# Kernel optimization log

Measured on AMD Instinct MI355X. Metric: run time of the kernel, lower is better.

The kernel has to match this reference:

```python
import jax, jax.numpy as jnp
import numpy as np

B, T, D, H, Dh, ROT = 2, 2048, 2048, 16, 128, 64
DFF = 4 * D
EPS = 1e-5
NEG = -1e9


def setup_inputs() -> dict:
    key = jax.random.key(0)
    ks = jax.random.split(key, 8)
    s = lambda k, shape, sc: jax.random.normal(k, shape, jnp.float32) * sc
    return {
        "x": s(ks[0], (B, T, D), 1.0),
        "ln_scale": jnp.ones((D,), jnp.float32),
        "ln_offset": jnp.zeros((D,), jnp.float32),
        "wq": s(ks[1], (D, D), 0.02),
        "wk": s(ks[2], (D, D), 0.02),
        "wv": s(ks[3], (D, D), 0.02),
        "wo": s(ks[4], (D, D), 0.02),
        "w1": s(ks[5], (D, DFF), 0.02),
        "b1": jnp.zeros((DFF,), jnp.float32),
        "w2": s(ks[6], (DFF, D), 0.02),
        "b2": jnp.zeros((D,), jnp.float32),
    }


def reference(x, ln_scale, ln_offset, wq, wk, wv, wo, w1, b1, w2, b2):
    def ln(h):  # ReplicatedLayerNorm, fp32 internal; note: same params used twice (shared self.norm)
        h32 = h.astype(jnp.float32)
        m = jnp.mean(h32, axis=-1, keepdims=True)
        v = jnp.var(h32, axis=-1, keepdims=True)
        y = (h32 - m) * jax.lax.rsqrt(v + EPS)
        return (y * ln_scale + ln_offset).astype(h.dtype)

    xn = ln(x)
    q = (xn @ wq).reshape(B, T, H, Dh)
    k = (xn @ wk).reshape(B, T, H, Dh)
    v = (xn @ wv).reshape(B, T, H, Dh)

    # GPT-J interleaved RoPE on first ROT dims
    pos = jnp.arange(T, dtype=jnp.float32)
    inv_freq = 1.0 / (10000.0 ** (jnp.arange(0, ROT, 2, dtype=jnp.float32) / ROT))
    freqs = pos[:, None] * inv_freq[None, :]            # (T, ROT/2)
    cos = jnp.repeat(jnp.cos(freqs), 2, axis=-1)[None, :, None, :]  # (1,T,1,ROT)
    sin = jnp.repeat(jnp.sin(freqs), 2, axis=-1)[None, :, None, :]

    def rope(t):
        tr, tp = t[..., :ROT], t[..., ROT:]
        x1 = tr[..., 0::2]
        x2 = tr[..., 1::2]
        rot_half = jnp.stack((-x2, x1), axis=-1).reshape(tr.shape)
        return jnp.concatenate([tr * cos + rot_half * sin, tp], axis=-1)

    q, k = rope(q), rope(k)

    scale = 1.0 / jnp.sqrt(jnp.float32(Dh))
    scores = jnp.einsum('bthd,bshd->bhts', q, k) * scale
    mask = jnp.where(jnp.tril(jnp.ones((T, T), bool)), 0.0, NEG).astype(scores.dtype)
    w = jax.nn.softmax(scores + mask, axis=-1)
    ctx = jnp.einsum('bhts,bshd->bthd', w, v).reshape(B, T, D)
    x1_ = x + ctx @ wo

    xn2 = ln(x1_)
    h = jax.nn.gelu(xn2.astype(jnp.float32) @ w1 + b1)  # default approximate gelu, as in source
    ff = (h @ w2 + b2).astype(x.dtype)
    return x1_ + ff
```

## Files before the change

### kernel.cpp

```cpp
#include <hip/hip_runtime.h>
#include <hip/hip_bf16.h>

#define B_   2
#define T_   2048
#define D_   2048
#define H_   16
#define DH_  128
#define DFF_ 8192

typedef __attribute__((ext_vector_type(8))) short bf16x8;
typedef __attribute__((ext_vector_type(4))) float f32x4;

__device__ __forceinline__ short f2bf(float f) {
    __hip_bfloat16 h = __float2bfloat16(f);
    return *reinterpret_cast<short*>(&h);
}

__device__ __forceinline__ void gload_lds16(const void* g, void* l) {
    __builtin_amdgcn_global_load_lds(
        (const __attribute__((address_space(1))) void*)g,
        (__attribute__((address_space(3))) void*)l,
        16, 0, 0);
}

__device__ __forceinline__ float gelu_tanh(float x) {
    float x3 = x * x * x;
    return 0.5f * x * (1.f + tanhf(0.7978845608028654f * (x + 0.044715f * x3)));
}

#define MFMA32(a, b, c) __builtin_amdgcn_mfma_f32_16x16x32_bf16((a), (b), (c), 0, 0, 0)

__global__ __launch_bounds__(256) void transpose_cvt(const float* __restrict__ in,
                                                     __hip_bfloat16* __restrict__ out,
                                                     int K, int N, int out_ld, int out_row0)
{
    __shared__ float t[32][65];
    const int n0 = blockIdx.x * 64, k0 = blockIdx.y * 32;
    const int tid = threadIdx.x;
    {
        int kr = tid >> 4;
        int nc = (tid & 15) * 4;
        const float* src = in + (size_t)(k0 + kr) * N + n0 + nc;
        float4 a = *reinterpret_cast<const float4*>(src);
        float4 b = *reinterpret_cast<const float4*>(src + (size_t)16 * N);
        t[kr][nc] = a.x; t[kr][nc + 1] = a.y; t[kr][nc + 2] = a.z; t[kr][nc + 3] = a.w;
        t[kr + 16][nc] = b.x; t[kr + 16][nc + 1] = b.y; t[kr + 16][nc + 2] = b.z; t[kr + 16][nc + 3] = b.w;
    }
    __syncthreads();
    {
        int n  = tid >> 2;
        int kc = (tid & 3) * 8;
        __hip_bfloat16 ob[8];
#pragma unroll
        for (int j = 0; j < 8; ++j) ob[j] = __float2bfloat16(t[kc + j][n]);
        *reinterpret_cast<uint4*>(out + (size_t)(out_row0 + n0 + n) * out_ld + k0 + kc) =
            *reinterpret_cast<uint4*>(ob);
    }
}

__global__ __launch_bounds__(256) void ln_kernel(const float* __restrict__ x,
                                                 const float* __restrict__ sc,
                                                 const float* __restrict__ of,
                                                 __hip_bfloat16* __restrict__ out)
{
    int row = blockIdx.x, tid = threadIdx.x;
    const float* xr = x + (size_t)row * D_;
    float4 v0 = reinterpret_cast<const float4*>(xr)[tid * 2];
    float4 v1 = reinterpret_cast<const float4*>(xr)[tid * 2 + 1];
    float vv[8] = {v0.x, v0.y, v0.z, v0.w, v1.x, v1.y, v1.z, v1.w};
    float s = 0.f, ss = 0.f;
#pragma unroll
    for (int j = 0; j < 8; ++j) { s += vv[j]; ss += vv[j] * vv[j]; }
    for (int o = 32; o; o >>= 1) { s += __shfl_down(s, o); ss += __shfl_down(ss, o); }
    __shared__ float red[8];
    int wid = tid >> 6, lane = tid & 63;
    if (!lane) { red[wid] = s; red[4 + wid] = ss; }
    __syncthreads();
    s  = red[0] + red[1] + red[2] + red[3];
    ss = red[4] + red[5] + red[6] + red[7];
    float mean = s * (1.f / D_);
    float var  = ss * (1.f / D_) - mean * mean;
    float rstd = rsqrtf(var + 1e-5f);
    int c0 = tid * 8;
    __hip_bfloat16 ob[8];
#pragma unroll
    for (int j = 0; j < 8; ++j)
        ob[j] = __float2bfloat16((vv[j] - mean) * rstd * sc[c0 + j] + of[c0 + j]);
    *reinterpret_cast<uint4*>(out + (size_t)row * D_ + c0) = *reinterpret_cast<uint4*>(ob);
}

template<int EPI, int BM>
__global__ __launch_bounds__(512, 2) void gemm8p(
    const __hip_bfloat16* __restrict__ A, const __hip_bfloat16* __restrict__ BT,
    void* __restrict__ Cout, const float* __restrict__ bias,
    const float* __restrict__ resid, int M, int N, int K)
{
    constexpr int MFR = BM / 32;
    constexpr int AUL = BM / 128;
    constexpr int VMC = AUL + 2;
    __shared__ short As[2 * 2 * BM * 32];
    __shared__ short Bs[2 * 2 * 256 * 32];

    const int tid = threadIdx.x;
    const int wid = tid >> 6, lane = tid & 63;
    const int lo = lane & 15, hi = lane >> 4;
    const int wr = wid >> 2, wc = wid & 3;

    const int gx = gridDim.x;
    const int nwg = gx * gridDim.y;
    const int bid = blockIdx.y * gx + blockIdx.x;
    const int swz = (bid & 7) * (nwg >> 3) + (bid >> 3);
    const int m0 = (swz / gx) * BM, n0 = (swz % gx) * 256;

    auto stageA = [&](int tt, int ks) {
#pragma unroll
        for (int l = 0; l < AUL; ++l) {
            int c    = l * 512 + tid;
            int row  = c >> 2, ksub = c & 3;
            int kc   = tt * 64 + ks * 32 + ((ksub ^ ((row >> 1) & 3)) << 3);
            int c0   = l * 512 + wid * 64;
            gload_lds16(A + (size_t)(m0 + row) * K + kc,
                        (char*)As + ((tt & 1) * 2 + ks) * (BM * 64) + c0 * 16);
        }
    };
    auto stageB = [&](int tt, int ks) {
#pragma unroll
        for (int l = 0; l < 2; ++l) {
            int c    = l * 512 + tid;
            int row  = c >> 2, ksub = c & 3;
            int kc   = tt * 64 + ks * 32 + ((ksub ^ ((row >> 1) & 3)) << 3);
            int c0   = l * 512 + wid * 64;
            gload_lds16(BT + (size_t)(n0 + row) * K + kc,
                        (char*)Bs + ((tt & 1) * 2 + ks) * 16384 + c0 * 16);
        }
    };

    const int fsw  = (hi ^ ((lo >> 1) & 3)) << 4;
    const int arow = wr * (BM / 2) + lo;
    const int brow = wc * 64 + lo;

    f32x4 acc[MFR][4] = {};
    const int NT = K >> 6;

    stageA(0, 0); stageB(0, 0); stageA(0, 1); stageB(0, 1);
    asm volatile("s_waitcnt vmcnt(%0)" :: "i"(VMC) : "memory");
    __builtin_amdgcn_s_barrier();

#define PHASE_MFMA(J)                                                         \
        __builtin_amdgcn_s_barrier();                                         \
        asm volatile("s_waitcnt lgkmcnt(0)" ::: "memory");                    \
        __builtin_amdgcn_s_setprio(1);                                        \
        _Pragma("unroll")                                                     \
        for (int m = 0; m < MFR; ++m) {                                       \
            acc[m][J]     = MFMA32(af[m], b0, acc[m][J]);                     \
            acc[m][J + 1] = MFMA32(af[m], b1, acc[m][J + 1]);                 \
        }                                                                     \
        __builtin_amdgcn_s_setprio(0);

#pragma unroll 2
    for (int t = 0; t < NT; ++t) {
        const int bsel = t & 1;
        const bool pf = (t + 1 < NT);
        const char* Ab = (const char*)As + bsel * (2 * BM * 64);
        const char* Bb = (const char*)Bs + bsel * 32768;
        bf16x8 af[MFR], b0, b1;

#pragma unroll
        for (int m = 0; m < MFR; ++m)
            af[m] = *reinterpret_cast<const bf16x8*>(Ab + (arow + m * 16) * 64 + fsw);
        b0 = *reinterpret_cast<const bf16x8*>(Bb + brow * 64 + fsw);
        b1 = *reinterpret_cast<const bf16x8*>(Bb + (brow + 16) * 64 + fsw);
        if (pf) stageA(t + 1, 0);
        PHASE_MFMA(0)
        __builtin_amdgcn_s_barrier();

        b0 = *reinterpret_cast<const bf16x8*>(Bb + (brow + 32) * 64 + fsw);
        b1 = *reinterpret_cast<const bf16x8*>(Bb + (brow + 48) * 64 + fsw);
        if (pf) stageB(t + 1, 0);
        PHASE_MFMA(2)
        asm volatile("s_waitcnt vmcnt(%0)" :: "i"(VMC) : "memory");
        __builtin_amdgcn_s_barrier();

#pragma unroll
        for (int m = 0; m < MFR; ++m)
            af[m] = *reinterpret_cast<const bf16x8*>(Ab + BM * 64 + (arow + m * 16) * 64 + fsw);
        b0 = *reinterpret_cast<const bf16x8*>(Bb + 16384 + brow * 64 + fsw);
        b1 = *reinterpret_cast<const bf16x8*>(Bb + 16384 + (brow + 16) * 64 + fsw);
        if (pf) stageA(t + 1, 1);
        PHASE_MFMA(0)
        __builtin_amdgcn_s_barrier();

        b0 = *reinterpret_cast<const bf16x8*>(Bb + 16384 + (brow + 32) * 64 + fsw);
        b1 = *reinterpret_cast<const bf16x8*>(Bb + 16384 + (brow + 48) * 64 + fsw);
        if (pf) stageB(t + 1, 1);
        PHASE_MFMA(2)
        asm volatile("s_waitcnt vmcnt(%0)" :: "i"(VMC) : "memory");
        __builtin_amdgcn_s_barrier();
    }
#undef PHASE_MFMA

    float* Cf = (float*)Cout;
    __hip_bfloat16* Cb = (__hip_bfloat16*)Cout;

    bool doRope = false;
    float invf[4];
    if (EPI == 4) {
        doRope = (n0 < 4096) && ((wc & 1) == 0);
        if (doRope) {
#pragma unroll
            for (int j = 0; j < 4; ++j) {
                int p = ((j >> 1) * 32 + (j & 1) * 16 + lo) >> 1;
                invf[j] = exp2f((float)p * -0.4152410118609203f);
            }
        }
    }

#pragma unroll
    for (int m = 0; m < MFR; ++m) {
        int rbase = m0 + wr * (BM / 2) + m * 16 + hi * 4;
#pragma unroll
        for (int j = 0; j < 4; ++j) {
            int col = n0 + wc * 64 + (j >> 1) * 32 + (j & 1) * 16 + lo;
            float bv = (EPI == 2 || EPI == 3) ? bias[col] : 0.f;
#pragma unroll
            for (int i = 0; i < 4; ++i) {
                size_t idx = (size_t)(rbase + i) * N + col;
                float v = acc[m][j][i];
                if (EPI == 4) {
                    if (doRope) {
                        float pv = __shfl_xor(v, 1);
                        int tt = (rbase + i) & (T_ - 1);
                        float fr = (float)tt * invf[j];
                        float cs, sn;
                        __sincosf(fr, &sn, &cs);
                        v = (lo & 1) ? (v * cs + pv * sn) : (v * cs - pv * sn);
                    }
                    Cb[idx] = __float2bfloat16(v);
                    continue;
                }
                if (EPI == 2 || EPI == 3) v += bv;
                if (EPI == 2) v = gelu_tanh(v);
                if (EPI == 1 || EPI == 3) v += resid[idx];
                if (EPI == 0 || EPI == 2) Cb[idx] = __float2bfloat16(v);
                else                      Cf[idx] = v;
            }
        }
    }
}

template<int EPI>
__global__ __launch_bounds__(512, 4) void gemmq(
    const __hip_bfloat16* __restrict__ A, const __hip_bfloat16* __restrict__ BT,
    void* __restrict__ Cout, const float* __restrict__ bias,
    const float* __restrict__ resid, int M, int N, int K)
{
    __shared__ short As[2 * 2 * 128 * 32];
    __shared__ short Bs[2 * 2 * 128 * 32];

    const int tid = threadIdx.x;
    const int wid = tid >> 6, lane = tid & 63;
    const int lo = lane & 15, hi = lane >> 4;
    const int wr = wid >> 1, wc = wid & 3;
    const int wr2 = wid >> 2;

    const int gx = gridDim.x;
    const int nwg = gx * gridDim.y;
    const int bid = blockIdx.y * gx + blockIdx.x;
    const int swz = (bid & 7) * (nwg >> 3) + (bid >> 3);
    const int m0 = (swz / gx) * 128, n0 = (swz % gx) * 128;

    const int srow = tid >> 2, sslot = tid & 3;
    auto stageA = [&](int tt, int ks) {
        int kc = tt * 64 + ks * 32 + ((sslot ^ ((srow >> 1) & 3)) << 3);
        gload_lds16(A + (size_t)(m0 + srow) * K + kc,
                    (char*)As + ((tt & 1) * 2 + ks) * 8192 + wid * 1024);
    };
    auto stageB = [&](int tt, int ks) {
        int kc = tt * 64 + ks * 32 + ((sslot ^ ((srow >> 1) & 3)) << 3);
        gload_lds16(BT + (size_t)(n0 + srow) * K + kc,
                    (char*)Bs + ((tt & 1) * 2 + ks) * 8192 + wid * 1024);
    };

    const int fsw  = (hi ^ ((lo >> 1) & 3)) << 4;
    const int arow = wr2 * 64 + lo;
    const int brow = wc * 32 + lo;

    f32x4 acc[4][2] = {};
    const int NT = K >> 6;

    stageA(0, 0); stageB(0, 0); stageA(0, 1); stageB(0, 1);
    asm volatile("s_waitcnt vmcnt(2)" ::: "memory");
    __builtin_amdgcn_s_barrier();

#pragma unroll 2
    for (int t = 0; t < NT; ++t) {
        const int bsel = t & 1;
        const bool pf = (t + 1 < NT);
        const char* Ab = (const char*)As + bsel * 16384;
        const char* Bb = (const char*)Bs + bsel * 16384;

#pragma unroll
        for (int ks = 0; ks < 2; ++ks) {
            bf16x8 af[4], b0, b1;
#pragma unroll
            for (int m = 0; m < 4; ++m)
                af[m] = *reinterpret_cast<const bf16x8*>(
                    Ab + ks * 8192 + (arow + m * 16) * 64 + fsw);
            b0 = *reinterpret_cast<const bf16x8*>(Bb + ks * 8192 + brow * 64 + fsw);
            b1 = *reinterpret_cast<const bf16x8*>(Bb + ks * 8192 + (brow + 16) * 64 + fsw);
            if (pf) { stageA(t + 1, ks); stageB(t + 1, ks); }
            asm volatile("s_waitcnt lgkmcnt(0)" ::: "memory");
            __builtin_amdgcn_s_setprio(1);
#pragma unroll
            for (int m = 0; m < 4; ++m) {
                acc[m][0] = MFMA32(af[m], b0, acc[m][0]);
                acc[m][1] = MFMA32(af[m], b1, acc[m][1]);
            }
            __builtin_amdgcn_s_setprio(0);
            if (pf) asm volatile("s_waitcnt vmcnt(2)" ::: "memory");
            else    asm volatile("s_waitcnt vmcnt(0)" ::: "memory");
            __builtin_amdgcn_s_barrier();
        }
    }

    float* Cf = (float*)Cout;
    __hip_bfloat16* Cb = (__hip_bfloat16*)Cout;
#pragma unroll
    for (int m = 0; m < 4; ++m) {
        int rbase = m0 + wr2 * 64 + m * 16 + hi * 4;
#pragma unroll
        for (int j = 0; j < 2; ++j) {
            int col = n0 + wc * 32 + j * 16 + lo;
            float bv = (EPI == 2 || EPI == 3) ? bias[col] : 0.f;
#pragma unroll
            for (int i = 0; i < 4; ++i) {
                size_t idx = (size_t)(rbase + i) * N + col;
                float v = acc[m][j][i];
                if (EPI == 2 || EPI == 3) v += bv;
                if (EPI == 2) v = gelu_tanh(v);
                if (EPI == 1 || EPI == 3) v += resid[idx];
                if (EPI == 0 || EPI == 2) Cb[idx] = __float2bfloat16(v);
                else                      Cf[idx] = v;
            }
        }
    }
}

__global__ __launch_bounds__(512) void attn_kernel(const __hip_bfloat16* __restrict__ qkv,
                                                   __hip_bfloat16* __restrict__ ctx)
{
    constexpr int LDQ = 3 * D_;
    constexpr int SV  = 68;

    int idx = blockIdx.y * 16 + blockIdx.x;
    int swz = (idx & 7) * 64 + (idx >> 3);
    const int bh  = swz >> 4;
    const int bxr = 15 - (swz & 15);
    const int b = bh >> 4, h = bh & 15;
    const int tq0 = bxr * 128;

    const int tid = threadIdx.x, wid = tid >> 6, lane = tid & 63;
    const int lo = lane & 15, hi = lane >> 4;
    const int t0 = tq0 + wid * 16;

    __shared__ short Ks[2][64 * 128];
    __shared__ short VsT[128 * SV];

    const __hip_bfloat16* qrow = qkv + (size_t)(b * T_ + t0 + lo) * LDQ + h * DH_;
    bf16x8 qf[4];
#pragma unroll
    for (int dk = 0; dk < 4; ++dk)
        qf[dk] = *reinterpret_cast<const bf16x8*>(qrow + dk * 32 + hi * 8);

    f32x4 octx[8] = {};
    float mreg = -1e30f, lreg = 0.f;

    const size_t kvrow0 = (size_t)(b * T_) * LDQ + h * DH_;
    const int nst = 2 * (bxr + 1);

    bf16x8 vr[2];

#define STAGE_K(s0v, buf)                                                     \
    do {                                                                      \
        _Pragma("unroll")                                                     \
        for (int i = 0; i < 2; ++i) {                                         \
            int c    = i * 512 + tid;                                         \
            int sr   = c >> 4;                                                \
            int cbs  = ((c & 15) * 16) ^ ((sr & 7) << 4);                     \
            gload_lds16(qkv + kvrow0 + (size_t)((s0v) + sr) * LDQ + D_ + (cbs >> 1), \
                        &Ks[buf][c * 8]);                                     \
        }                                                                     \
    } while (0)

#define LOAD_V(s0v)                                                           \
    do {                                                                      \
        _Pragma("unroll")                                                     \
        for (int it = 0; it < 2; ++it) {                                      \
            int c = it * 512 + tid;                                           \
            int s = c >> 4, dc = c & 15;                                      \
            vr[it] = *reinterpret_cast<const bf16x8*>(                        \
                qkv + kvrow0 + (size_t)((s0v) + s) * LDQ + 2 * D_ + dc * 8);  \
        }                                                                     \
    } while (0)

    STAGE_K(0, 0);
    LOAD_V(0);

    for (int st = 0; st < nst; ++st) {
        const int s0 = st * 64;
        const int cur = st & 1;
        __syncthreads();

#pragma unroll
        for (int it = 0; it < 2; ++it) {
            int c = it * 512 + tid;
            int s = c >> 4, dc = c & 15;
            int sswz = s ^ ((dc & 15) << 2);
            short* dst = &VsT[(dc * 8) * SV + sswz];
#pragma unroll
            for (int j = 0; j < 8; ++j)
                dst[j * SV] = vr[it][j];
        }
        if (st + 1 < nst) {
            STAGE_K(s0 + 64, cur ^ 1);
            LOAD_V(s0 + 64);
        }
        asm volatile("s_waitcnt lgkmcnt(0)" ::: "memory");
        __builtin_amdgcn_s_barrier();
        __builtin_amdgcn_sched_barrier(0);

        f32x4 sfr[4] = {};
        __builtin_amdgcn_s_setprio(1);
#pragma unroll
        for (int f = 0; f < 4; ++f) {
            int srow = f * 16 + lo;
            int sw = (srow & 7) << 4;
#pragma unroll
            for (int dk = 0; dk < 4; ++dk) {
                bf16x8 kf = *reinterpret_cast<const bf16x8*>(
                    (const char*)&Ks[cur][0] + srow * 256 + ((dk * 64 + hi * 16) ^ sw));
                sfr[f] = MFMA32(kf, qf[dk], sfr[f]);
            }
        }
        __builtin_amdgcn_s_setprio(0);

        const float qsc = 0.08838834764831845f;
#pragma unroll
        for (int f = 0; f < 4; ++f)
#pragma unroll
            for (int i = 0; i < 4; ++i)
                sfr[f][i] *= qsc;
        if (st >= nst - 2) {
#pragma unroll
            for (int f = 0; f < 4; ++f)
#pragma unroll
                for (int i = 0; i < 4; ++i)
                    if (s0 + f * 16 + hi * 4 + i > t0 + lo) sfr[f][i] = -1e30f;
        }

        float mx = -1e30f;
#pragma unroll
        for (int f = 0; f < 4; ++f)
#pragma unroll
            for (int i = 0; i < 4; ++i)
                mx = fmaxf(mx, sfr[f][i]);
        mx = fmaxf(mx, __shfl_xor(mx, 16));
        mx = fmaxf(mx, __shfl_xor(mx, 32));

        if (!__all(mx - mreg <= 8.f)) {
            float mn = fmaxf(mreg, mx);
            float ps = __expf(mreg - mn);
            mreg = mn;
            lreg *= ps;
            float psq[4];
#pragma unroll
            for (int i = 0; i < 4; ++i)
                psq[i] = __shfl(ps, hi * 4 + i);
#pragma unroll
            for (int f8 = 0; f8 < 8; ++f8)
#pragma unroll
                for (int i = 0; i < 4; ++i)
                    octx[f8][i] *= psq[i];
        }

        float sum = 0.f;
#pragma unroll
        for (int f = 0; f < 4; ++f)
#pragma unroll
            for (int i = 0; i < 4; ++i) {
                sfr[f][i] = __expf(sfr[f][i] - mreg);
                sum += sfr[f][i];
            }
        sum += __shfl_xor(sum, 16);
        sum += __shfl_xor(sum, 32);
        lreg += sum;

#pragma unroll
        for (int ks = 0; ks < 2; ++ks) {
            union { bf16x8 v; short s[8]; } pa;
#pragma unroll
            for (int j = 0; j < 4; ++j) {
                pa.s[j]     = f2bf(sfr[2 * ks][j]);
                pa.s[j + 4] = f2bf(sfr[2 * ks + 1][j]);
            }
            __builtin_amdgcn_s_setprio(1);
#pragma unroll
            for (int f8 = 0; f8 < 8; ++f8) {
                int d = f8 * 16 + lo;
                int sw2 = ((d >> 3) & 15) << 2;
                const short* vrow = &VsT[d * SV];
                union { bf16x8 v; uint2 u[2]; } vb;
                vb.u[0] = *reinterpret_cast<const uint2*>(vrow + ((ks * 32 + hi * 4) ^ sw2));
                vb.u[1] = *reinterpret_cast<const uint2*>(vrow + ((ks * 32 + 16 + hi * 4) ^ sw2));
                octx[f8] = MFMA32(pa.v, vb.v, octx[f8]);
            }
            __builtin_amdgcn_s_setprio(0);
        }
    }
#undef STAGE_K
#undef LOAD_V

    float linv[4];
#pragma unroll
    for (int i = 0; i < 4; ++i)
        linv[i] = 1.f / __shfl(lreg, hi * 4 + i);
#pragma unroll
    for (int i = 0; i < 4; ++i) {
        size_t rb = (size_t)(b * T_ + t0 + hi * 4 + i) * D_ + h * DH_;
#pragma unroll
        for (int f8 = 0; f8 < 8; ++f8)
            ctx[rb + f8 * 16 + lo] = __float2bfloat16(octx[f8][i] * linv[i]);
    }
}

extern "C" void kernel_launch(void* const* d_in, const int* in_sizes, int n_in,
                              void* d_out, int out_size, void* d_ws, size_t ws_size,
                              hipStream_t stream)
{
    (void)in_sizes; (void)n_in; (void)out_size; (void)ws_size;
    const float* x   = (const float*)d_in[0];
    const float* lns = (const float*)d_in[1];
    const float* lno = (const float*)d_in[2];
    const float* wq  = (const float*)d_in[3];
    const float* wk  = (const float*)d_in[4];
    const float* wv  = (const float*)d_in[5];
    const float* wo  = (const float*)d_in[6];
    const float* w1  = (const float*)d_in[7];
    const float* b1  = (const float*)d_in[8];
    const float* w2  = (const float*)d_in[9];
    const float* b2  = (const float*)d_in[10];
    float* out = (float*)d_out;

    char* ws = (char*)d_ws;
    __hip_bfloat16* wqkvT = (__hip_bfloat16*)(ws);
    __hip_bfloat16* woT   = (__hip_bfloat16*)(ws + 25165824);
    __hip_bfloat16* w1T   = (__hip_bfloat16*)(ws + 33554432);
    __hip_bfloat16* w2T   = (__hip_bfloat16*)(ws + 67108864);
    __hip_bfloat16* xn    = (__hip_bfloat16*)(ws + 100663296);
    __hip_bfloat16* qkv   = (__hip_bfloat16*)(ws + 117440512);
    __hip_bfloat16* hbuf  = qkv;
    __hip_bfloat16* ctx   = (__hip_bfloat16*)(ws + 167772160);
    float*          x1    = (float*)(ws + 184549376);

    transpose_cvt<<<dim3(32, 64),  256, 0, stream>>>(wq, wqkvT, 2048, 2048, 2048, 0);
    transpose_cvt<<<dim3(32, 64),  256, 0, stream>>>(wk, wqkvT, 2048, 2048, 2048, 2048);
    transpose_cvt<<<dim3(32, 64),  256, 0, stream>>>(wv, wqkvT, 2048, 2048, 2048, 4096);
    transpose_cvt<<<dim3(32, 64),  256, 0, stream>>>(wo, woT,   2048, 2048, 2048, 0);
    transpose_cvt<<<dim3(128, 64), 256, 0, stream>>>(w1, w1T,   2048, 8192, 2048, 0);
    transpose_cvt<<<dim3(32, 256), 256, 0, stream>>>(w2, w2T,   8192, 2048, 8192, 0);

    ln_kernel<<<4096, 256, 0, stream>>>(x, lns, lno, xn);
    gemm8p<4, 128><<<dim3(24, 32), 512, 0, stream>>>(xn, wqkvT, qkv, nullptr, nullptr, 4096, 6144, 2048);
    attn_kernel<<<dim3(16, 32), 512, 0, stream>>>(qkv, ctx);
    gemmq<1><<<dim3(16, 32), 512, 0, stream>>>(ctx, woT, x1, nullptr, x, 4096, 2048, 2048);
    ln_kernel<<<4096, 256, 0, stream>>>(x1, lns, lno, xn);
    gemm8p<2, 256><<<dim3(32, 16), 512, 0, stream>>>(xn, w1T, hbuf, b1, nullptr, 4096, 8192, 2048);
    gemmq<3><<<dim3(16, 32), 512, 0, stream>>>(hbuf, w2T, out, b2, x1, 4096, 2048, 8192);
}
```

Before: 721.8 us.

## Stage V via direct-to-LDS loads and read with transposing LDS reads

The attention kernel now double-buffers V in LDS through global_load_lds, as it already does for K. The PV operand is read with ds_read_b64_tr_b16 transposing LDS reads, which replaces the register round-trip and the manual scatter-transpose into a padded VsT buffer. This also removes an extra barrier per tile. Separately, the four square weight transposes are merged into one launch with a z-dimension. The cost is more LDS (a second 16KB buffer) and hand-written inline asm with an explicit lgkmcnt wait before the MFMAs. Correctness depends on the staging layout matching the transpose-read semantics.

```diff
diff --git a/kernel.cpp b/kernel.cpp
--- a/kernel.cpp
+++ b/kernel.cpp
@@ -54,6 +54,39 @@
 #pragma unroll
         for (int j = 0; j < 8; ++j) ob[j] = __float2bfloat16(t[kc + j][n]);
         *reinterpret_cast<uint4*>(out + (size_t)(out_row0 + n0 + n) * out_ld + k0 + kc) =
+            *reinterpret_cast<uint4*>(ob);
+    }
+}
+
+__global__ __launch_bounds__(256) void transpose_cvt4(
+    const float* __restrict__ wq, const float* __restrict__ wk,
+    const float* __restrict__ wv, const float* __restrict__ wo,
+    __hip_bfloat16* __restrict__ oqkv, __hip_bfloat16* __restrict__ owo)
+{
+    const int z = blockIdx.z;
+    const float* in = (z == 0) ? wq : (z == 1) ? wk : (z == 2) ? wv : wo;
+    __hip_bfloat16* out = (z < 3) ? (oqkv + (size_t)z * 2048 * 2048) : owo;
+
+    __shared__ float t[32][65];
+    const int n0 = blockIdx.x * 64, k0 = blockIdx.y * 32;
+    const int tid = threadIdx.x;
+    {
+        int kr = tid >> 4;
+        int nc = (tid & 15) * 4;
+        const float* src = in + (size_t)(k0 + kr) * 2048 + n0 + nc;
+        float4 a = *reinterpret_cast<const float4*>(src);
+        float4 b = *reinterpret_cast<const float4*>(src + (size_t)16 * 2048);
+        t[kr][nc] = a.x; t[kr][nc + 1] = a.y; t[kr][nc + 2] = a.z; t[kr][nc + 3] = a.w;
+        t[kr + 16][nc] = b.x; t[kr + 16][nc + 1] = b.y; t[kr + 16][nc + 2] = b.z; t[kr + 16][nc + 3] = b.w;
+    }
+    __syncthreads();
+    {
+        int n  = tid >> 2;
+        int kc = (tid & 3) * 8;
+        __hip_bfloat16 ob[8];
+#pragma unroll
+        for (int j = 0; j < 8; ++j) ob[j] = __float2bfloat16(t[kc + j][n]);
+        *reinterpret_cast<uint4*>(out + (size_t)(n0 + n) * 2048 + k0 + kc) =
             *reinterpret_cast<uint4*>(ob);
     }
 }
@@ -260,7 +293,7 @@
     const int tid = threadIdx.x;
     const int wid = tid >> 6, lane = tid & 63;
     const int lo = lane & 15, hi = lane >> 4;
-    const int wr = wid >> 1, wc = wid & 3;
+    const int wc = wid & 3;
     const int wr2 = wid >> 2;
 
     const int gx = gridDim.x;
@@ -350,7 +383,6 @@
                                                    __hip_bfloat16* __restrict__ ctx)
 {
     constexpr int LDQ = 3 * D_;
-    constexpr int SV  = 68;
 
     int idx = blockIdx.y * 16 + blockIdx.x;
     int swz = (idx & 7) * 64 + (idx >> 3);
@@ -364,7 +396,7 @@
     const int t0 = tq0 + wid * 16;
 
     __shared__ short Ks[2][64 * 128];
-    __shared__ short VsT[128 * SV];
+    __shared__ short Vs[2][64 * 128];
 
     const __hip_bfloat16* qrow = qkv + (size_t)(b * T_ + t0 + lo) * LDQ + h * DH_;
     bf16x8 qf[4];
@@ -378,7 +410,8 @@
     const size_t kvrow0 = (size_t)(b * T_) * LDQ + h * DH_;
     const int nst = 2 * (bxr + 1);
 
-    bf16x8 vr[2];
+    const uint vbase0 = (uint)(size_t)(__attribute__((address_space(3))) short*)&Vs[0][0]
+                      + (uint)lane * 8u;
 
 #define STAGE_K(s0v, buf)                                                     \
     do {                                                                      \
@@ -392,42 +425,30 @@
         }                                                                     \
     } while (0)
 
-#define LOAD_V(s0v)                                                           \
+#define STAGE_V(s0v, buf)                                                     \
     do {                                                                      \
         _Pragma("unroll")                                                     \
-        for (int it = 0; it < 2; ++it) {                                      \
-            int c = it * 512 + tid;                                           \
-            int s = c >> 4, dc = c & 15;                                      \
-            vr[it] = *reinterpret_cast<const bf16x8*>(                        \
-                qkv + kvrow0 + (size_t)((s0v) + s) * LDQ + 2 * D_ + dc * 8);  \
+        for (int i = 0; i < 2; ++i) {                                         \
+            int c  = i * 512 + tid;                                           \
+            int s  = ((c >> 3) & 15) * 4 + ((c >> 1) & 3);                    \
+            int d0 = (c >> 7) * 16 + (c & 1) * 8;                             \
+            gload_lds16(qkv + kvrow0 + (size_t)((s0v) + s) * LDQ + 2 * D_ + d0, \
+                        &Vs[buf][c * 8]);                                     \
         }                                                                     \
     } while (0)
 
     STAGE_K(0, 0);
-    LOAD_V(0);
+    STAGE_V(0, 0);
 
     for (int st = 0; st < nst; ++st) {
         const int s0 = st * 64;
         const int cur = st & 1;
         __syncthreads();
 
-#pragma unroll
-        for (int it = 0; it < 2; ++it) {
-            int c = it * 512 + tid;
-            int s = c >> 4, dc = c & 15;
-            int sswz = s ^ ((dc & 15) << 2);
-            short* dst = &VsT[(dc * 8) * SV + sswz];
-#pragma unroll
-            for (int j = 0; j < 8; ++j)
-                dst[j * SV] = vr[it][j];
-        }
         if (st + 1 < nst) {
             STAGE_K(s0 + 64, cur ^ 1);
-            LOAD_V(s0 + 64);
-        }
-        asm volatile("s_waitcnt lgkmcnt(0)" ::: "memory");
-        __builtin_amdgcn_s_barrier();
-        __builtin_amdgcn_sched_barrier(0);
+            STAGE_V(s0 + 64, cur ^ 1);
+        }
 
         f32x4 sfr[4] = {};
         __builtin_amdgcn_s_setprio(1);
@@ -495,6 +516,7 @@
         sum += __shfl_xor(sum, 32);
         lreg += sum;
 
+        const uint vaddr = vbase0 + (uint)(cur << 14);
 #pragma unroll
         for (int ks = 0; ks < 2; ++ks) {
             union { bf16x8 v; short s[8]; } pa;
@@ -503,22 +525,31 @@
                 pa.s[j]     = f2bf(sfr[2 * ks][j]);
                 pa.s[j + 4] = f2bf(sfr[2 * ks + 1][j]);
             }
+            unsigned long long tr[8][2];
+#pragma unroll
+            for (int f8 = 0; f8 < 8; ++f8) {
+                asm volatile("ds_read_b64_tr_b16 %0, %2 offset:%3\n\t"
+                             "ds_read_b64_tr_b16 %1, %2 offset:%4"
+                             : "=&v"(tr[f8][0]), "=&v"(tr[f8][1])
+                             : "v"(vaddr),
+                               "i"((f8 * 16 + 8 * ks) * 128),
+                               "i"((f8 * 16 + 8 * ks + 4) * 128));
+            }
+            asm volatile("s_waitcnt lgkmcnt(0)" ::: "memory");
+            __builtin_amdgcn_sched_barrier(0);
             __builtin_amdgcn_s_setprio(1);
 #pragma unroll
             for (int f8 = 0; f8 < 8; ++f8) {
-                int d = f8 * 16 + lo;
-                int sw2 = ((d >> 3) & 15) << 2;
-                const short* vrow = &VsT[d * SV];
-                union { bf16x8 v; uint2 u[2]; } vb;
-                vb.u[0] = *reinterpret_cast<const uint2*>(vrow + ((ks * 32 + hi * 4) ^ sw2));
-                vb.u[1] = *reinterpret_cast<const uint2*>(vrow + ((ks * 32 + 16 + hi * 4) ^ sw2));
+                union { bf16x8 v; unsigned long long q[2]; } vb;
+                vb.q[0] = tr[f8][0];
+                vb.q[1] = tr[f8][1];
                 octx[f8] = MFMA32(pa.v, vb.v, octx[f8]);
             }
             __builtin_amdgcn_s_setprio(0);
         }
     }
 #undef STAGE_K
-#undef LOAD_V
+#undef STAGE_V
 
     float linv[4];
 #pragma unroll
@@ -562,12 +593,9 @@
     __hip_bfloat16* ctx   = (__hip_bfloat16*)(ws + 167772160);
     float*          x1    = (float*)(ws + 184549376);
 
-    transpose_cvt<<<dim3(32, 64),  256, 0, stream>>>(wq, wqkvT, 2048, 2048, 2048, 0);
-    transpose_cvt<<<dim3(32, 64),  256, 0, stream>>>(wk, wqkvT, 2048, 2048, 2048, 2048);
-    transpose_cvt<<<dim3(32, 64),  256, 0, stream>>>(wv, wqkvT, 2048, 2048, 2048, 4096);
-    transpose_cvt<<<dim3(32, 64),  256, 0, stream>>>(wo, woT,   2048, 2048, 2048, 0);
-    transpose_cvt<<<dim3(128, 64), 256, 0, stream>>>(w1, w1T,   2048, 8192, 2048, 0);
-    transpose_cvt<<<dim3(32, 256), 256, 0, stream>>>(w2, w2T,   8192, 2048, 8192, 0);
+    transpose_cvt4<<<dim3(32, 64, 4), 256, 0, stream>>>(wq, wk, wv, wo, wqkvT, woT);
+    transpose_cvt<<<dim3(128, 64), 256, 0, stream>>>(w1, w1T, 2048, 8192, 2048, 0);
+    transpose_cvt<<<dim3(32, 256), 256, 0, stream>>>(w2, w2T, 8192, 2048, 8192, 0);
 
     ln_kernel<<<4096, 256, 0, stream>>>(x, lns, lno, xn);
     gemm8p<4, 128><<<dim3(24, 32), 512, 0, stream>>>(xn, wqkvT, qkv, nullptr, nullptr, 4096, 6144, 2048);
```

Result: faster. 685.7 us (-5.0%).
